# Performance work log

Measured on AMD Instinct MI355X. Metric: run time of the kernel, lower is better.

Reference implementation:

```python
import jax, jax.numpy as jnp
import numpy as np
from functools import partial

# Config (BranchNet 'big'-style)
HIST = [42, 78, 150, 294, 582]
PW = [3, 6, 12, 24, 48]
SHIFTING = [False, False, True, True, True]
CW = 7          # conv width
F = 32          # conv filters
E = 32          # embedding dims
B = 4096        # batch
H_TOT = 590     # total history length
V = 8192        # 2**(pc_hash_bits+1)
WBITS = 2       # weight quantization bits
ABITS = 3       # activation quantization bits
EPS = 1e-5


@partial(jax.custom_vjp, nondiff_argnums=(1,))
def quant_signed(x, bits):
    # Quantize.forward (signed, bits>1): round(x*scale)/scale, scale=(1<<(bits-1))-1
    scale = float((1 << (bits - 1)) - 1)
    return jnp.round(x * scale) / scale

def _q_fwd(x, bits):
    return quant_signed(x, bits), None

def _q_bwd(bits, res, g):
    # straight-through estimator, matching Quantize.backward
    return (g,)

quant_signed.defvjp(_q_fwd, _q_bwd)


def batchnorm(x, gamma, beta, axes, pshape):
    # training-mode BatchNorm1d: batch statistics, biased variance
    m = jnp.mean(x, axis=axes, keepdims=True)
    v = jnp.var(x, axis=axes, keepdims=True)
    return gamma.reshape(pshape) * (x - m) * jax.lax.rsqrt(v + EPS) + beta.reshape(pshape)


def extract_slice_history(x, global_shift, slice_size, pooling_width, shifting):
    # vectorized version of the per-sample Python loop in extract_slice_history
    h_tot = x.shape[1]
    if shifting:
        s = jnp.mod(global_shift, pooling_width)              # [B]
        start = (h_tot - s - slice_size)[:, None]             # [B,1]
        idx = start + jnp.arange(slice_size)[None, :]         # [B,L]
        return jnp.take_along_axis(x, idx, axis=1)
    return x[:, -slice_size:]


def fc_layer(x, W, b, gamma, beta):
    # FCLayer with quantized weights + batchnorm + hardtanh + quantized act
    w = quant_signed(jnp.clip(W, -1.0, 1.0), WBITS)
    y = x @ w.T + b
    y = batchnorm(y, gamma, beta, (0,), (1, -1))
    y = jnp.clip(y, -1.0, 1.0)  # hardtanh
    return quant_signed(y, ABITS)


def branchnet_forward(x, global_shift, emb, conv_w, conv_b, bn1_g, bn1_b,
                      bnp_g, bnp_b, W1, b1, g1, be1, W2, b2, g2, be2, W3, b3):
    feats = []
    for i in range(len(HIST)):
        L, pw = HIST[i], PW[i]
        xs = extract_slice_history(x, global_shift, L, pw, SHIFTING[i])  # [B,L] int
        e = jnp.take(emb[i], xs, axis=0)                                 # [B,L,E]
        e = jnp.transpose(e, (0, 2, 1))                                  # [B,E,L]
        h = jax.lax.conv_general_dilated(
            e, conv_w[i], window_strides=(1,), padding='VALID',
            dimension_numbers=('NCH', 'OIH', 'NCH')) + conv_b[i][None, :, None]
        h = batchnorm(h, bn1_g[i], bn1_b[i], (0, 2), (1, -1, 1))
        h = jnp.tanh(h)
        T = (L - CW + 1) // pw                                           # = 12
        p = h[:, :, :T * pw].reshape(h.shape[0], F, T, pw).mean(axis=-1) # AvgPool1d
        p = batchnorm(p, bnp_g[i], bnp_b[i], (0, 2), (1, -1, 1))
        feats.append(p.reshape(p.shape[0], -1))                          # [B, F*T]
    z = jnp.concatenate(feats, axis=1)                                   # [B, 1920]
    z = fc_layer(z, W1, b1, g1, be1)
    z = fc_layer(z, W2, b2, g2, be2)
    w3 = quant_signed(jnp.clip(W3, -1.0, 1.0), WBITS)
    out = z @ w3.T + b3                                                  # [B,1]
    return out[:, 0]                                                     # squeeze(dim=1)


def setup_inputs() -> dict:
    key = jax.random.key(0)
    ks = jax.random.split(key, 12)
    return {
        'x': jax.random.randint(ks[0], (B, H_TOT), 0, V, dtype=jnp.int32),
        'global_shift': jax.random.randint(ks[1], (B,), 0, 48, dtype=jnp.int32),
        'emb': jax.random.normal(ks[2], (5, V, E), jnp.float32) * 0.1,
        'conv_w': jax.random.normal(ks[3], (5, F, E, CW), jnp.float32) * 0.1,
        'conv_b': jax.random.normal(ks[4], (5, F), jnp.float32) * 0.01,
        'bn1_g': jnp.ones((5, F), jnp.float32),
        'bn1_b': jnp.zeros((5, F), jnp.float32),
        'bnp_g': jnp.ones((5, F), jnp.float32),
        'bnp_b': jnp.zeros((5, F), jnp.float32),
        'W1': jax.random.uniform(ks[5], (2048, 1920), jnp.float32, -1.0, 1.0),
        'b1': jax.random.normal(ks[6], (2048,), jnp.float32) * 0.01,
        'g1': jnp.ones((2048,), jnp.float32),
        'be1': jnp.zeros((2048,), jnp.float32),
        'W2': jax.random.uniform(ks[7], (2048, 2048), jnp.float32, -1.0, 1.0),
        'b2': jax.random.normal(ks[8], (2048,), jnp.float32) * 0.01,
        'g2': jnp.ones((2048,), jnp.float32),
        'be2': jnp.zeros((2048,), jnp.float32),
        'W3': jax.random.uniform(ks[9], (1, 2048), jnp.float32, -1.0, 1.0),
        'b3': jax.random.normal(ks[10], (1,), jnp.float32) * 0.01,
    }


def reference(x, global_shift, emb, conv_w, conv_b, bn1_g, bn1_b, bnp_g, bnp_b,
              W1, b1, g1, be1, W2, b2, g2, be2, W3, b3):
    return branchnet_forward(x, global_shift, emb, conv_w, conv_b, bn1_g, bn1_b,
                             bnp_g, bnp_b, W1, b1, g1, be1, W2, b2, g2, be2, W3, b3)
```

## Files before the change

### kernel.cpp

```cpp
#include <hip/hip_runtime.h>
#include <cmath>

#define HTOT  590
#define BATCH 4096
#define VOCAB 8192

typedef _Float16 f16;
typedef __attribute__((ext_vector_type(8))) _Float16 f16x8;
typedef __attribute__((ext_vector_type(4))) _Float16 f16x4;
typedef __attribute__((ext_vector_type(4))) float f32x4;
typedef __attribute__((ext_vector_type(16))) float f32x16;

constexpr size_t OFF_EHL  = 0;
constexpr size_t OFF_WF   = 1310720;
constexpr size_t OFF_PA   = 1364480;
constexpr size_t OFF_PB   = 2937344;
constexpr size_t OFF_BN1  = 4510208;
constexpr size_t OFF_BNP  = 4510528;
constexpr size_t OFF_CP   = 4510848;
constexpr size_t OFF_BNF1 = 4641920;
constexpr size_t OFF_PRAW = 4646016;
constexpr size_t OFF_W1P  = 12510336;
constexpr size_t OFF_W2P  = 14476416;
constexpr size_t OFF_Y    = 16573568;
constexpr size_t OFF_BNF2 = 24962176;
constexpr size_t OFF_Z2K  = 0;
constexpr size_t OFF_Z3K  = 4194304;

__device__ __forceinline__ float qw(float w) {
  return rintf(fminf(fmaxf(w, -1.f), 1.f));
}
__device__ __forceinline__ float4 ld4(const float* p) {
  return *reinterpret_cast<const float4*>(p);
}
__device__ __forceinline__ float tanh_c(float u) {
  const float e = __expf(2.f*u);
  return 1.f - __fdividef(2.f, e + 1.f);
}

#define MF(A,B,C) __builtin_amdgcn_mfma_f32_32x32x16_f16(A,B,C,0,0,0)
#define WV(K,KS,V) (*reinterpret_cast<const f16x8*>(wfsl + (((K)*2+(KS))*3+(V))*256 + lane*4))

__global__ __launch_bounds__(256) void k_eprep(const float* __restrict__ emb,
                                               f16* __restrict__ ehl)
{
  const int idx = blockIdx.x*256 + threadIdx.x;
  const int c = idx & 31, v = (idx >> 5) & 8191, slice = idx >> 18;
  const float val = emb[(size_t)(slice*VOCAB + v)*32 + c];
  const f16 hi = (f16)val;
  const f16 lo = (f16)((val - (float)hi)*2048.f);
  f16* row = ehl + (size_t)(slice*VOCAB + v)*64;
  row[c] = hi; row[32 + c] = lo;
}

__global__ __launch_bounds__(256) void k_wfprep(const float* __restrict__ convw,
                                                f16* __restrict__ wf)
{
  const int idx = blockIdx.x*256 + threadIdx.x;
  const int j = idx & 7, lane = (idx >> 3) & 63;
  const int rest = idx >> 9;
  const int v = rest % 3;
  const int rest2 = rest / 3;
  const int ks = rest2 & 1, kk = rest2 >> 1;
  const int k = kk % 7, slice = kk / 7;
  const int f = lane & 31, c = ks*16 + (lane >> 5)*8 + j;
  const float val = convw[((slice*32 + f)*32 + c)*7 + k];
  const f16 hi = (f16)val;
  f16 o;
  if (v == 0)      o = (f16)((float)hi * 2048.f);
  else if (v == 1) o = (f16)((val - (float)hi)*2048.f);
  else             o = hi;
  wf[idx] = o;
}

template<int PASS>
__global__ __launch_bounds__(256, 4) void k_convm(const int* __restrict__ x,
                                                  const int* __restrict__ gshift,
                                                  const float* __restrict__ ehl,
                                                  const float* __restrict__ wfrag,
                                                  const float* __restrict__ bn1,
                                                  float* __restrict__ z,
                                                  float* __restrict__ partials)
{
  const int b = blockIdx.x;
  const int type = blockIdx.y;
  const int tid = threadIdx.x;
  const int wid = tid >> 6, lane = tid & 63;
  const int lt = lane & 31, hf = lane >> 5;

  __shared__ float smem[9408];
  __shared__ int   tokid[294];

  float* tokarr = smem;
  f16*   hstat  = (f16*)smem;
  float* part2  = smem + 6000;
  float* thbuf  = smem;
  float* poolb  = smem + 4224;

  const int gsv = gshift[b];
  const int NTOK = (type == 0) ? 270 : 294;

  for (int i = tid; i < NTOK; i += 256) {
    int xs, q = i;
    if (type == 0) {
      if (i < 42)       { xs = 548; }
      else if (i < 120) { xs = 512; q = i - 42; }
      else              { xs = 440 - gsv % 12; q = i - 120; }
    } else if (type == 1) xs = 296 - gsv % 24;
    else if (type == 2)   xs = 8 - gsv % 48;
    else                  xs = 8 - gsv % 48 + 288;
    int xi = xs + q; if (xi < 0) xi += HTOT;
    tokid[i] = x[b*HTOT + xi];
  }
  __syncthreads();
  for (int j = tid; j < NTOK*8; j += 256) {
    const int row = j >> 3, ch = j & 7;
    const int sl = (type == 0) ? (row < 42 ? 0 : (row < 120 ? 1 : 2)) : ((type == 1) ? 3 : 4);
    const float4 v = ld4(ehl + (size_t)(sl*VOCAB + tokid[row])*32 + ch*4);
    *reinterpret_cast<float4*>(&tokarr[ch*1176 + row*4]) = v;
  }
  __syncthreads();

  int slice, tb, nt, slotoff, ThV, pw, si;
  if (type == 0) {
    if      (wid == 0) { slice=0; tb=0;  nt=2; slotoff=0;   ThV=36;  pw=3;  si=0; }
    else if (wid == 1) { slice=1; tb=0;  nt=3; slotoff=42;  ThV=72;  pw=6;  si=1; }
    else if (wid == 2) { slice=2; tb=0;  nt=3; slotoff=120; ThV=144; pw=12; si=2; }
    else               { slice=2; tb=96; nt=2; slotoff=120; ThV=144; pw=12; si=2; }
  } else if (type == 1) {
    slice=3; pw=24; ThV=288; slotoff=0; si=0;
    tb = (wid == 0) ? 0 : 32 + wid*64; nt = (wid == 0) ? 3 : 2;
  } else if (type == 2) {
    slice=4; pw=48; ThV=288; slotoff=0; si=0;
    tb = (wid == 0) ? 0 : 32 + wid*64; nt = (wid == 0) ? 3 : 2;
  } else {
    slice=4; pw=48; ThV=576; slotoff=-288; si=0;
    tb = 288 + ((wid == 0) ? 0 : 32 + wid*64); nt = (wid == 0) ? 3 : 2;
  }
  const int wb = (type == 3) ? 6 : 0;
  const int slot0 = (type == 0) ? ((wid == 0) ? 0 : (wid == 1) ? 2 : (wid == 2) ? 5 : 8)
                                : ((wid == 0) ? 0 : 1 + wid*2);

  const float* wfsl = wfrag + slice*10752;

  f32x16 acc[3];
  #pragma unroll
  for (int r = 0; r < 3; ++r)
    #pragma unroll
    for (int i = 0; i < 16; ++i) acc[r][i] = 0.f;

  const float* pb = tokarr + hf*1176 + (size_t)(slotoff + tb + lt)*4;
  #pragma unroll 1
  for (int k = 0; k < 7; ++k) {
    const f16x8 wh2_0 = WV(k,0,0), wl_0 = WV(k,0,1), wh_0 = WV(k,0,2);
    const f16x8 wh2_1 = WV(k,1,0), wl_1 = WV(k,1,1), wh_1 = WV(k,1,2);
    #pragma unroll
    for (int r = 0; r < 3; ++r) if (r < nt) {
      const float* rp = pb + k*4 + r*128;
      const f16x8 bh0 = *(const f16x8*)(rp);
      const f16x8 bh1 = *(const f16x8*)(rp + 2352);
      const f16x8 bl0 = *(const f16x8*)(rp + 4704);
      const f16x8 bl1 = *(const f16x8*)(rp + 7056);
      acc[r] = MF(wh2_0, bh0, acc[r]);
      acc[r] = MF(wl_0,  bh0, acc[r]);
      acc[r] = MF(wh_0,  bl0, acc[r]);
      acc[r] = MF(wh2_1, bh1, acc[r]);
      acc[r] = MF(wl_1,  bh1, acc[r]);
      acc[r] = MF(wh_1,  bl1, acc[r]);
    }
  }
  __syncthreads();

  if (PASS == 0) {
    #pragma unroll
    for (int r = 0; r < 3; ++r) if (r < nt) {
      const int tbg = tb + r*32;
      const int slot = slot0 + r;
      #pragma unroll
      for (int i = 0; i < 16; ++i) {
        const int fr = (i&3) + 8*(i>>2) + 4*hf;
        const float h = acc[r][i]*(1.f/2048.f);
        const float hv = (tbg + lt < ThV) ? h : 0.f;
        hstat[slot*1088 + fr*34 + lt] = (f16)hv;
      }
    }
    __syncthreads();
    const int nslot = (type == 0) ? 10 : 9;
    for (int j = tid; j < nslot*32; j += 256) {
      const int slot = j >> 5, f = j & 31;
      const f16* rowp = hstat + slot*1088 + f*34;
      float s1 = 0.f, s2 = 0.f;
      #pragma unroll
      for (int t = 0; t < 32; ++t) { const float v = (float)rowp[t]; s1 += v; s2 += v*v; }
      part2[(slot*32 + f)*2]     = s1;
      part2[(slot*32 + f)*2 + 1] = s2;
    }
    __syncthreads();
    const int nch = (type == 0) ? 96 : 32;
    if (tid < nch) {
      const int sic = tid >> 5, f = tid & 31;
      int slo, shi, Pb;
      if (type == 0) {
        slo = (sic == 0) ? 0 : (sic == 1) ? 2 : 5;
        shi = (sic == 0) ? 2 : (sic == 1) ? 5 : 10;
        Pb  = sic*32;
      } else { slo = 0; shi = 9; Pb = 96 + (type - 1)*32; }
      float s1 = 0.f, s2 = 0.f;
      for (int s = slo; s < shi; ++s) {
        s1 += part2[(s*32 + f)*2];
        s2 += part2[(s*32 + f)*2 + 1];
      }
      partials[(size_t)b*384 + (Pb + f)*2]     = s1;
      partials[(size_t)b*384 + (Pb + f)*2 + 1] = s2;
    }
    return;
  }

  for (int i = tid; i < 2304; i += 256) poolb[i] = 0.f;
  __syncthreads();

  float A1v[16], B1v[16];
  #pragma unroll
  for (int i = 0; i < 16; ++i) {
    const int fr = (i&3) + 8*(i>>2) + 4*hf;
    A1v[i] = bn1[slice*32 + fr];
    B1v[i] = bn1[160 + slice*32 + fr];
  }

  #pragma unroll
  for (int r = 0; r < 3; ++r) if (r < nt) {
    const int tbg = tb + r*32;
    #pragma unroll
    for (int i = 0; i < 16; ++i) {
      const int fr = (i&3) + 8*(i>>2) + 4*hf;
      const float h = acc[r][i]*(1.f/2048.f);
      thbuf[wid*1056 + fr*33 + lt] = tanh_c(A1v[i]*h + B1v[i]);
    }
    const int tvend = min(tbg + 32, ThV);
    const int wlo = tbg / pw, whi = (tvend - 1) / pw;
    for (int w = wlo; w <= whi; ++w) {
      const int lo = max(w*pw, tbg), hi2 = min((w+1)*pw, tvend);
      float s = 0.f;
      for (int t = lo + hf; t < hi2; t += 2) s += thbuf[wid*1056 + lt*33 + (t - tbg)];
      s += __shfl_xor(s, 32);
      if (hf == 0) {
        const int piece = (w*pw < tbg) ? 1 : 0;
        poolb[(si*12 + (w - wb))*64 + piece*32 + lt] = s;
      }
    }
  }
  __syncthreads();

  const int nch = (type == 0) ? 96 : 32;
  if (tid < nch) {
    const int sic = tid >> 5, f = tid & 31;
    const int sg = (type == 0) ? sic : ((type == 1) ? 3 : 4);
    const int P = (sg < 4) ? sg*32 + f : ((type == 2) ? 128 + f : 160 + f);
    const int pwc = (type == 0) ? ((sic == 0) ? 3 : (sic == 1) ? 6 : 12)
                                : ((type == 1) ? 24 : 48);
    const int nwin = (type >= 2) ? 6 : 12;
    const int wbc = (type == 3) ? 6 : 0;
    const float inv = 1.f/(float)pwc;
    float s1 = 0.f, s2 = 0.f;
    for (int wl = 0; wl < nwin; ++wl) {
      const float p = (poolb[(sic*12 + wl)*64 + f] + poolb[(sic*12 + wl)*64 + 32 + f]) * inv;
      z[(size_t)b*1920 + sg*384 + (wl + wbc)*32 + f] = p;
      s1 += p; s2 += p*p;
    }
    partials[(size_t)b*384 + P*2]     = s1;
    partials[(size_t)b*384 + P*2 + 1] = s2;
  }
}

template<int PASS>
__global__ __launch_bounds__(256) void k_bnfinal(const float* __restrict__ partials,
                                                 const float* __restrict__ gamma,
                                                 const float* __restrict__ beta,
                                                 float* __restrict__ outAB)
{
  const int c = blockIdx.x;
  const int slice = c >> 5, f = c & 31;
  const int tid = threadIdx.x;
  double s1 = 0.0, s2 = 0.0;
  for (int b = tid; b < BATCH; b += 256) {
    const float* p = partials + (size_t)b*384;
    if (slice < 4) { s1 += p[(slice*32+f)*2]; s2 += p[(slice*32+f)*2+1]; }
    else {
      s1 += (double)p[(128+f)*2]   + (double)p[(160+f)*2];
      s2 += (double)p[(128+f)*2+1] + (double)p[(160+f)*2+1];
    }
  }
  __shared__ double r1[256], r2[256];
  r1[tid] = s1; r2[tid] = s2;
  __syncthreads();
  for (int off = 128; off > 0; off >>= 1) {
    if (tid < off) { r1[tid] += r1[tid+off]; r2[tid] += r2[tid+off]; }
    __syncthreads();
  }
  if (tid == 0) {
    long N;
    if (PASS == 0) { const long Tall[5] = {36,72,144,288,576}; N = (long)BATCH * Tall[slice]; }
    else           { N = (long)BATCH * 12; }
    const double m   = r1[0]/(double)N;
    const double var = r2[0]/(double)N - m*m;
    const float rstd = (float)(1.0/sqrt(var + 1e-5));
    const float Aa = gamma[c]*rstd;
    outAB[c]       = Aa;
    outAB[160 + c] = beta[c] - Aa*(float)m;
  }
}

__global__ __launch_bounds__(256) void k_znorm(float* __restrict__ zz,
                                               const float* __restrict__ bnp)
{
  const size_t i4 = (size_t)blockIdx.x*256 + threadIdx.x;
  const float4 v = ld4(zz + i4*4);
  const int j = (int)((i4*4) % 1920);
  const int slice = j / 384, f0 = j & 31;
  const float4 A = ld4(bnp + slice*32 + f0);
  const float4 B = ld4(bnp + 160 + slice*32 + f0);
  const float zn[4] = {v.x*A.x+B.x, v.y*A.y+B.y, v.z*A.z+B.z, v.w*A.w+B.w};
  uint4 pk;
  unsigned w[4];
  #pragma unroll
  for (int e = 0; e < 4; ++e) {
    const f16 hi = (f16)zn[e];
    const f16 lo = (f16)(zn[e] - (float)hi);
    w[e] = (unsigned)__builtin_bit_cast(unsigned short, hi)
         | ((unsigned)__builtin_bit_cast(unsigned short, lo) << 16);
  }
  pk.x = w[0]; pk.y = w[1]; pk.z = w[2]; pk.w = w[3];
  *reinterpret_cast<uint4*>(zz + i4*4) = pk;
}

__global__ __launch_bounds__(256) void k_wprep1(const float* __restrict__ W1,
                                                f16* __restrict__ W1p)
{
  const int idx = blockIdx.x*256 + threadIdx.x;
  const int n = idx / 1920, klds = idx - n*1920;
  const int slice = klds / 384, r = klds - slice*384;
  const int tp = r >> 5, f = r & 31;
  W1p[idx] = (f16)qw(W1[n*1920 + slice*384 + f*12 + tp]);
}

__global__ __launch_bounds__(256) void k_wprep2(const float* __restrict__ W2,
                                                f16* __restrict__ W2p)
{
  const size_t i4 = (size_t)blockIdx.x*256 + threadIdx.x;
  const float4 v = ld4(W2 + i4*4);
  f16x4 o;
  o[0] = (f16)qw(v.x); o[1] = (f16)qw(v.y); o[2] = (f16)qw(v.z); o[3] = (f16)qw(v.w);
  *reinterpret_cast<f16x4*>(&W2p[i4*4]) = o;
}

template<int SPLIT, int PACKED>
__global__ __launch_bounds__(256) void k_mfgemm(const f16* __restrict__ Ahi,
                                               const unsigned* __restrict__ Apk,
                                               const f16* __restrict__ Bp,
                                               float* __restrict__ C,
                                               float* __restrict__ cpart,
                                               const int K, const float oscale)
{
  __shared__ f16 sA[(SPLIT+1)*128][40];
  __shared__ f16 sB[128][40];
  __shared__ float cst[4][4][16][2];
  const int tid = threadIdx.x;
  const int bm = blockIdx.y*128, bn = blockIdx.x*128;
  const int wid = tid >> 6, lane = tid & 63;
  const int wm = (wid >> 1)*64, wn = (wid & 1)*64;
  const int lgrp = lane >> 4, lrow = lane & 15;
  f32x4 acc[4][4];
  #pragma unroll
  for (int m = 0; m < 4; ++m)
    #pragma unroll
    for (int n = 0; n < 4; ++n) acc[m][n] = (f32x4){0.f,0.f,0.f,0.f};

  const int srow = tid >> 2, sc = (tid & 3)*8;
  for (int k0 = 0; k0 < K; k0 += 32) {
    #pragma unroll
    for (int u = 0; u < 2; ++u) {
      const int row = srow + u*64;
      if (PACKED) {
        const unsigned* ap = Apk + (size_t)(bm+row)*K + k0 + sc;
        const uint4 v0 = *reinterpret_cast<const uint4*>(ap);
        const uint4 v1 = *reinterpret_cast<const uint4*>(ap + 4);
        uint4 hi, lo;
        hi.x = (v0.x & 0xffffu) | (v0.y << 16);  hi.y = (v0.z & 0xffffu) | (v0.w << 16);
        hi.z = (v1.x & 0xffffu) | (v1.y << 16);  hi.w = (v1.z & 0xffffu) | (v1.w << 16);
        lo.x = (v0.x >> 16) | (v0.y & 0xffff0000u);  lo.y = (v0.z >> 16) | (v0.w & 0xffff0000u);
        lo.z = (v1.x >> 16) | (v1.y & 0xffff0000u);  lo.w = (v1.z >> 16) | (v1.w & 0xffff0000u);
        *reinterpret_cast<uint4*>(&sA[row][sc])     = hi;
        *reinterpret_cast<uint4*>(&sA[128+row][sc]) = lo;
      } else {
        const uint4 va = *reinterpret_cast<const uint4*>(&Ahi[(size_t)(bm+row)*K + k0 + sc]);
        *reinterpret_cast<uint4*>(&sA[row][sc]) = va;
      }
      const uint4 vb = *reinterpret_cast<const uint4*>(&Bp[(size_t)(bn+row)*K + k0 + sc]);
      *reinterpret_cast<uint4*>(&sB[row][sc]) = vb;
    }
    __syncthreads();
    f16x8 bf[4];
    #pragma unroll
    for (int n = 0; n < 4; ++n)
      bf[n] = *reinterpret_cast<const f16x8*>(&sB[wn + n*16 + lrow][lgrp*8]);
    #pragma unroll
    for (int m = 0; m < 4; ++m) {
      const f16x8 ah = *reinterpret_cast<const f16x8*>(&sA[wm + m*16 + lrow][lgrp*8]);
      #pragma unroll
      for (int n = 0; n < 4; ++n)
        acc[m][n] = __builtin_amdgcn_mfma_f32_16x16x32_f16(ah, bf[n], acc[m][n], 0, 0, 0);
      if (SPLIT) {
        const f16x8 al = *reinterpret_cast<const f16x8*>(&sA[128 + wm + m*16 + lrow][lgrp*8]);
        #pragma unroll
        for (int n = 0; n < 4; ++n)
          acc[m][n] = __builtin_amdgcn_mfma_f32_16x16x32_f16(al, bf[n], acc[m][n], 0, 0, 0);
      }
    }
    __syncthreads();
  }
  float s1[4] = {0,0,0,0}, s2[4] = {0,0,0,0};
  #pragma unroll
  for (int m = 0; m < 4; ++m)
    #pragma unroll
    for (int n = 0; n < 4; ++n) {
      const int col = bn + wn + n*16 + lrow;
      #pragma unroll
      for (int r = 0; r < 4; ++r) {
        const float v = acc[m][n][r]*oscale;
        C[(size_t)(bm + wm + m*16 + lgrp*4 + r)*2048 + col] = v;
        s1[n] += v; s2[n] += v*v;
      }
    }
  #pragma unroll
  for (int n = 0; n < 4; ++n) {
    s1[n] += __shfl_xor(s1[n], 16); s1[n] += __shfl_xor(s1[n], 32);
    s2[n] += __shfl_xor(s2[n], 16); s2[n] += __shfl_xor(s2[n], 32);
  }
  if (lgrp == 0) {
    #pragma unroll
    for (int n = 0; n < 4; ++n) { cst[wid][n][lrow][0] = s1[n]; cst[wid][n][lrow][1] = s2[n]; }
  }
  __syncthreads();
  if (tid < 128) {
    const int n = tid >> 5, half = (tid >> 4) & 1, lr = tid & 15;
    const float a1 = cst[half][n][lr][0] + cst[half+2][n][lr][0];
    const float a2 = cst[half][n][lr][1] + cst[half+2][n][lr][1];
    const int col = bn + half*64 + n*16 + lr;
    cpart[(size_t)col*64 + blockIdx.y*2]     = a1;
    cpart[(size_t)col*64 + blockIdx.y*2 + 1] = a2;
  }
}

__global__ __launch_bounds__(256) void k_colfinal(const float* __restrict__ part,
                                                  const float* __restrict__ gamma,
                                                  const float* __restrict__ beta,
                                                  float* __restrict__ bnfc, int N)
{
  const int c = blockIdx.x*256 + threadIdx.x;
  if (c >= N) return;
  double s1 = 0.0, s2 = 0.0;
  #pragma unroll
  for (int ch = 0; ch < 32; ++ch) {
    s1 += (double)part[(size_t)c*64 + ch*2];
    s2 += (double)part[(size_t)c*64 + ch*2 + 1];
  }
  const double m   = s1/4096.0;
  const double var = s2/4096.0 - m*m;
  const float rstd = (float)(1.0/sqrt(var + 1e-5));
  const float Aa = gamma[c]*rstd;
  bnfc[c]        = Aa;
  bnfc[2048 + c] = beta[c] - Aa*(float)m;
}

__global__ __launch_bounds__(256) void k_act(const float* __restrict__ Y,
                                             const float* __restrict__ bnfc,
                                             f16* __restrict__ Zk)
{
  const size_t i4 = (size_t)blockIdx.x*256 + threadIdx.x;
  const int cbase = (int)((i4*4) & 2047);
  const float4 v = ld4(Y + i4*4);
  const float4 A = ld4(bnfc + cbase);
  const float4 B = ld4(bnfc + 2048 + cbase);
  const float t[4] = {v.x*A.x+B.x, v.y*A.y+B.y, v.z*A.z+B.z, v.w*A.w+B.w};
  f16x4 o;
  #pragma unroll
  for (int e = 0; e < 4; ++e) {
    const float c = fminf(fmaxf(t[e], -1.f), 1.f);
    o[e] = (f16)rintf(c*3.f);
  }
  *reinterpret_cast<f16x4*>(&Zk[i4*4]) = o;
}

__global__ __launch_bounds__(256) void k_final(const f16* __restrict__ Z3,
                                               const float* __restrict__ W3,
                                               const float* __restrict__ b3,
                                               float* __restrict__ out)
{
  const int b = blockIdx.x;
  const int tid = threadIdx.x;
  float s = 0.f;
  for (int j = tid; j < 2048; j += 256)
    s += (float)Z3[(size_t)b*2048 + j] * qw(W3[j]);
  __shared__ float red[256];
  red[tid] = s;
  __syncthreads();
  for (int off = 128; off > 0; off >>= 1) {
    if (tid < off) red[tid] += red[tid+off];
    __syncthreads();
  }
  if (tid == 0) out[b] = red[0]*(1.f/3.f) + b3[0];
}

extern "C" void kernel_launch(void* const* d_in, const int* in_sizes, int n_in,
                              void* d_out, int out_size, void* d_ws, size_t ws_size,
                              hipStream_t stream)
{
  const int*   x    = (const int*)d_in[0];
  const int*   gs   = (const int*)d_in[1];
  const float* emb  = (const float*)d_in[2];
  const float* cw   = (const float*)d_in[3];
  const float* bn1g = (const float*)d_in[5];
  const float* bn1b = (const float*)d_in[6];
  const float* bnpg = (const float*)d_in[7];
  const float* bnpb = (const float*)d_in[8];
  const float* W1   = (const float*)d_in[9];
  const float* g1   = (const float*)d_in[11];
  const float* be1  = (const float*)d_in[12];
  const float* W2   = (const float*)d_in[13];
  const float* g2   = (const float*)d_in[15];
  const float* be2  = (const float*)d_in[16];
  const float* W3   = (const float*)d_in[17];
  const float* b3   = (const float*)d_in[18];
  float* ws  = (float*)d_ws;
  float* out = (float*)d_out;

  k_eprep<<<5120, 256, 0, stream>>>(emb, (f16*)(ws + OFF_EHL));
  k_wfprep<<<420, 256, 0, stream>>>(cw, (f16*)(ws + OFF_WF));

  k_convm<0><<<dim3(BATCH, 4), 256, 0, stream>>>(x, gs, ws + OFF_EHL, ws + OFF_WF,
                                                 ws + OFF_BN1, nullptr, ws + OFF_PA);
  k_bnfinal<0><<<160, 256, 0, stream>>>(ws + OFF_PA, bn1g, bn1b, ws + OFF_BN1);
  k_convm<1><<<dim3(BATCH, 4), 256, 0, stream>>>(x, gs, ws + OFF_EHL, ws + OFF_WF,
                                                 ws + OFF_BN1, ws + OFF_PRAW, ws + OFF_PB);
  k_bnfinal<1><<<160, 256, 0, stream>>>(ws + OFF_PB, bnpg, bnpb, ws + OFF_BNP);
  k_znorm<<<7680, 256, 0, stream>>>(ws + OFF_PRAW, ws + OFF_BNP);
  k_wprep1<<<15360, 256, 0, stream>>>(W1, (f16*)(ws + OFF_W1P));
  k_wprep2<<<4096, 256, 0, stream>>>(W2, (f16*)(ws + OFF_W2P));

  k_mfgemm<1,1><<<dim3(16, 32), 256, 0, stream>>>(nullptr, (const unsigned*)(ws + OFF_PRAW),
                                                  (const f16*)(ws + OFF_W1P),
                                                  ws + OFF_Y, ws + OFF_CP, 1920, 1.f);
  k_colfinal<<<8, 256, 0, stream>>>(ws + OFF_CP, g1, be1, ws + OFF_BNF1, 2048);
  k_act<<<8192, 256, 0, stream>>>(ws + OFF_Y, ws + OFF_BNF1, (f16*)(ws + OFF_Z2K));

  k_mfgemm<0,0><<<dim3(16, 32), 256, 0, stream>>>((const f16*)(ws + OFF_Z2K), nullptr,
                                                  (const f16*)(ws + OFF_W2P),
                                                  ws + OFF_Y, ws + OFF_CP, 2048, 1.f/3.f);
  k_colfinal<<<8, 256, 0, stream>>>(ws + OFF_CP, g2, be2, ws + OFF_BNF2, 2048);
  k_act<<<8192, 256, 0, stream>>>(ws + OFF_Y, ws + OFF_BNF2, (f16*)(ws + OFF_Z3K));

  k_final<<<4096, 256, 0, stream>>>((const f16*)(ws + OFF_Z3K), W3, b3, out);
}
```

Measured before the change: 766.2 us.

## Merge prep kernels, precompute token offsets, drop pool buffer zeroing

Merges the embedding and conv-weight prep kernels into one launch that branches on block index. In the conv kernel it stores precomputed embedding row offsets per token rather than recomputing the slice per load. It also removes the separate zero-fill pass and barrier on the pooling buffer, writing a zero into the second piece only when a window finishes inside the current tile. The aim is to trim launch overhead and per-block setup; the cost is that correctness now depends on every pooling slot being written by one of these paths.

```diff
diff --git a/kernel.cpp b/kernel.cpp
--- a/kernel.cpp
+++ b/kernel.cpp
@@ -41,36 +41,38 @@
 #define MF(A,B,C) __builtin_amdgcn_mfma_f32_32x32x16_f16(A,B,C,0,0,0)
 #define WV(K,KS,V) (*reinterpret_cast<const f16x8*>(wfsl + (((K)*2+(KS))*3+(V))*256 + lane*4))
 
-__global__ __launch_bounds__(256) void k_eprep(const float* __restrict__ emb,
-                                               f16* __restrict__ ehl)
-{
-  const int idx = blockIdx.x*256 + threadIdx.x;
-  const int c = idx & 31, v = (idx >> 5) & 8191, slice = idx >> 18;
-  const float val = emb[(size_t)(slice*VOCAB + v)*32 + c];
-  const f16 hi = (f16)val;
-  const f16 lo = (f16)((val - (float)hi)*2048.f);
-  f16* row = ehl + (size_t)(slice*VOCAB + v)*64;
-  row[c] = hi; row[32 + c] = lo;
-}
-
-__global__ __launch_bounds__(256) void k_wfprep(const float* __restrict__ convw,
-                                                f16* __restrict__ wf)
-{
-  const int idx = blockIdx.x*256 + threadIdx.x;
-  const int j = idx & 7, lane = (idx >> 3) & 63;
-  const int rest = idx >> 9;
-  const int v = rest % 3;
-  const int rest2 = rest / 3;
-  const int ks = rest2 & 1, kk = rest2 >> 1;
-  const int k = kk % 7, slice = kk / 7;
-  const int f = lane & 31, c = ks*16 + (lane >> 5)*8 + j;
-  const float val = convw[((slice*32 + f)*32 + c)*7 + k];
-  const f16 hi = (f16)val;
-  f16 o;
-  if (v == 0)      o = (f16)((float)hi * 2048.f);
-  else if (v == 1) o = (f16)((val - (float)hi)*2048.f);
-  else             o = hi;
-  wf[idx] = o;
+__global__ __launch_bounds__(256) void k_prep(const float* __restrict__ emb,
+                                              const float* __restrict__ convw,
+                                              f16* __restrict__ ehl,
+                                              f16* __restrict__ wf)
+{
+  const int bid = blockIdx.x;
+  const int tid = threadIdx.x;
+  if (bid < 5120) {
+    const int idx = bid*256 + tid;
+    const int c = idx & 31, v = (idx >> 5) & 8191, slice = idx >> 18;
+    const float val = emb[(size_t)(slice*VOCAB + v)*32 + c];
+    const f16 hi = (f16)val;
+    const f16 lo = (f16)((val - (float)hi)*2048.f);
+    f16* row = ehl + (size_t)(slice*VOCAB + v)*64;
+    row[c] = hi; row[32 + c] = lo;
+  } else {
+    const int idx = (bid - 5120)*256 + tid;
+    const int j = idx & 7, lane = (idx >> 3) & 63;
+    const int rest = idx >> 9;
+    const int v = rest % 3;
+    const int rest2 = rest / 3;
+    const int ks = rest2 & 1, kk = rest2 >> 1;
+    const int k = kk % 7, slice = kk / 7;
+    const int f = lane & 31, c = ks*16 + (lane >> 5)*8 + j;
+    const float val = convw[((slice*32 + f)*32 + c)*7 + k];
+    const f16 hi = (f16)val;
+    f16 o;
+    if (v == 0)      o = (f16)((float)hi * 2048.f);
+    else if (v == 1) o = (f16)((val - (float)hi)*2048.f);
+    else             o = hi;
+    wf[idx] = o;
+  }
 }
 
 template<int PASS>
@@ -89,7 +91,7 @@
   const int lt = lane & 31, hf = lane >> 5;
 
   __shared__ float smem[9408];
-  __shared__ int   tokid[294];
+  __shared__ int   tokoff[294];
 
   float* tokarr = smem;
   f16*   hstat  = (f16*)smem;
@@ -101,22 +103,21 @@
   const int NTOK = (type == 0) ? 270 : 294;
 
   for (int i = tid; i < NTOK; i += 256) {
-    int xs, q = i;
+    int xs, q = i, sl;
     if (type == 0) {
-      if (i < 42)       { xs = 548; }
-      else if (i < 120) { xs = 512; q = i - 42; }
-      else              { xs = 440 - gsv % 12; q = i - 120; }
-    } else if (type == 1) xs = 296 - gsv % 24;
-    else if (type == 2)   xs = 8 - gsv % 48;
-    else                  xs = 8 - gsv % 48 + 288;
+      if (i < 42)       { xs = 548; sl = 0; }
+      else if (i < 120) { xs = 512; q = i - 42; sl = 1; }
+      else              { xs = 440 - gsv % 12; q = i - 120; sl = 2; }
+    } else if (type == 1) { xs = 296 - gsv % 24; sl = 3; }
+    else if (type == 2)   { xs = 8 - gsv % 48; sl = 4; }
+    else                  { xs = 8 - gsv % 48 + 288; sl = 4; }
     int xi = xs + q; if (xi < 0) xi += HTOT;
-    tokid[i] = x[b*HTOT + xi];
+    tokoff[i] = (sl*VOCAB + x[b*HTOT + xi])*32;
   }
   __syncthreads();
   for (int j = tid; j < NTOK*8; j += 256) {
     const int row = j >> 3, ch = j & 7;
-    const int sl = (type == 0) ? (row < 42 ? 0 : (row < 120 ? 1 : 2)) : ((type == 1) ? 3 : 4);
-    const float4 v = ld4(ehl + (size_t)(sl*VOCAB + tokid[row])*32 + ch*4);
+    const float4 v = ld4(ehl + tokoff[row] + ch*4);
     *reinterpret_cast<float4*>(&tokarr[ch*1176 + row*4]) = v;
   }
   __syncthreads();
@@ -216,9 +217,6 @@
     return;
   }
 
-  for (int i = tid; i < 2304; i += 256) poolb[i] = 0.f;
-  __syncthreads();
-
   float A1v[16], B1v[16];
   #pragma unroll
   for (int i = 0; i < 16; ++i) {
@@ -246,6 +244,8 @@
       if (hf == 0) {
         const int piece = (w*pw < tbg) ? 1 : 0;
         poolb[(si*12 + (w - wb))*64 + piece*32 + lt] = s;
+        if (piece == 0 && (w+1)*pw <= tvend)
+          poolb[(si*12 + (w - wb))*64 + 32 + lt] = 0.f;
       }
     }
   }
@@ -534,8 +534,7 @@
   float* ws  = (float*)d_ws;
   float* out = (float*)d_out;
 
-  k_eprep<<<5120, 256, 0, stream>>>(emb, (f16*)(ws + OFF_EHL));
-  k_wfprep<<<420, 256, 0, stream>>>(cw, (f16*)(ws + OFF_WF));
+  k_prep<<<5540, 256, 0, stream>>>(emb, cw, (f16*)(ws + OFF_EHL), (f16*)(ws + OFF_WF));
 
   k_convm<0><<<dim3(BATCH, 4), 256, 0, stream>>>(x, gs, ws + OFF_EHL, ws + OFF_WF,
                                                  ws + OFF_BN1, nullptr, ws + OFF_PA);
```

Result: no change. 759.0 us, median of 2 (-0.9%).
